# Optimization experiments

Hardware: AMD Instinct MI355X
Metric: run time of the kernel (lower is better)

Reference implementation:

```python
import jax, jax.numpy as jnp
import numpy as np

B, T, C, A, P = 16, 1024, 512, 4096, 256  # batch, frames, phones, allophone arcs, phonemes


def setup_inputs() -> dict:
    key = jax.random.key(0)
    k1, k2, k3 = jax.random.split(key, 3)
    hs_pad = jax.random.normal(k1, (B, T, C), dtype=jnp.float32)
    # each phone has exactly A // C allophone arcs (full coverage, balanced)
    phone_arc_labels = jnp.arange(A, dtype=jnp.int32) % C
    arcs_per_phone = A // C
    # weights near -log(arcs_per_phone) so sum_a exp(log_prob + w) ~= 1,
    # matching a trained allophone layer and keeping the redis step log-safe
    alloW = 0.01 * jax.random.normal(k2, (A,), dtype=jnp.float32) - jnp.log(
        jnp.float32(arcs_per_phone)
    )
    phoneme_arc_labels = jax.random.randint(k3, (A,), 0, P, dtype=jnp.int32)
    return {
        "hs_pad": hs_pad,
        "alloW": alloW,
        "phone_arc_labels": phone_arc_labels,
        "phoneme_arc_labels": phoneme_arc_labels,
        "n_phonemes": P,
    }


def reference(hs_pad, alloW, phone_arc_labels, phoneme_arc_labels, n_phonemes):
    # log_softmax over phones
    log_probs = jax.nn.log_softmax(hs_pad, axis=-1)  # [B,T,C]
    # WFST intersection of linear emission graph with 1-state allophone graph:
    # arc a gets weight log_probs[..., phone_label(a)] + alloW[a]
    new_emissions = log_probs[..., phone_arc_labels] + alloW  # [B,T,A]
    # squash many phones per phoneme: exp + scatter-add over output labels
    ex = jnp.exp(new_emissions)
    Bq, Tq = ex.shape[0], ex.shape[1]
    squashed = jnp.zeros((Bq, Tq, n_phonemes), dtype=ex.dtype)
    squashed = squashed.at[..., phoneme_arc_labels].add(ex)  # [B,T,P]
    # redistribute probability mass so it sums to 1
    redistributed = (squashed.sum(axis=-1) - 1.0)[..., None] / n_phonemes
    squashed = squashed - redistributed
    return jnp.log(squashed)
```

## Files before the change

### kernel.cpp

```cpp
#include <hip/hip_runtime.h>
#include <hip/hip_bf16.h>

#define BT   16384
#define CDIM 512
#define ADIM 4096
#define PDIM 256

typedef __attribute__((ext_vector_type(8))) short short8;
typedef __attribute__((ext_vector_type(4))) float f32x4;

__device__ __forceinline__ unsigned short bf16_rne(float f) {
    unsigned int u = __float_as_uint(f);
    u += 0x7FFFu + ((u >> 16) & 1u);
    return (unsigned short)(u >> 16);
}

__global__ __launch_bounds__(256) void build_Wf(const float* __restrict__ alloW,
                                                const int* __restrict__ phone_lab,
                                                const int* __restrict__ phoneme_lab,
                                                unsigned short* __restrict__ Wf) {
    __shared__ float wrow[PDIM];
    const int c = blockIdx.x;
    const int t = threadIdx.x;
    wrow[t] = 0.0f;
    __syncthreads();
#pragma unroll
    for (int i = 0; i < ADIM / 256; ++i) {
        int a = i * 256 + t;
        if (phone_lab[a] == c)
            atomicAdd(&wrow[phoneme_lab[a]], __expf(alloW[a]));
    }
    __syncthreads();
    Wf[(c >> 5) * (PDIM * 32) + t * 32 + (c & 31)] = bf16_rne(wrow[t]);
}

__global__ __launch_bounds__(256) void allo_fused(const float* __restrict__ hs,
                                                  const unsigned short* __restrict__ Wf,
                                                  float* __restrict__ out) {
    __shared__ __align__(16) unsigned short Af[2 * 16 * 16 * 32];
    __shared__ float invZ[32];
    __shared__ float psum[4][32];

    const int tid  = threadIdx.x;
    const int row0 = blockIdx.x * 32;

    {
        const int r   = tid >> 3;
        const int ksl = tid & 7;
        const int rb  = r >> 4;
        const int cc  = r & 15;
        const float* hsr = hs + (size_t)(row0 + r) * CDIM + ksl * 4;
        unsigned short* af = Af + rb * 8192 + cc * 32 + ksl * 4;

        float s = 0.0f;
#pragma unroll
        for (int i = 0; i < 16; ++i) {
            float4 v = *(const float4*)(hsr + i * 32);
            float e0 = __expf(v.x), e1 = __expf(v.y);
            float e2 = __expf(v.z), e3 = __expf(v.w);
            s += (e0 + e1) + (e2 + e3);
            ushort4 pk;
            pk.x = bf16_rne(e0); pk.y = bf16_rne(e1);
            pk.z = bf16_rne(e2); pk.w = bf16_rne(e3);
            *(ushort4*)(af + i * 512) = pk;
        }
        s += __shfl_xor(s, 1);
        s += __shfl_xor(s, 2);
        s += __shfl_xor(s, 4);
        if (ksl == 0) invZ[r] = 1.0f / s;
    }
    __syncthreads();

    const int wave = tid >> 6;
    const int lane = tid & 63;
    const int c    = lane & 15;
    const int q    = lane >> 4;

    f32x4 acc[2][4];
#pragma unroll
    for (int rb = 0; rb < 2; ++rb)
#pragma unroll
        for (int cb = 0; cb < 4; ++cb)
            acc[rb][cb] = (f32x4){0.f, 0.f, 0.f, 0.f};

    const unsigned short* wb  = Wf + (size_t)(wave * 64 + c) * 32 + q * 8;
    const unsigned short* af0 = Af + c * 32 + q * 8;

#pragma unroll 4
    for (int kb = 0; kb < 16; ++kb) {
        short8 a0 = *(const short8*)(af0 + kb * 512);
        short8 a1 = *(const short8*)(af0 + 8192 + kb * 512);

        const unsigned short* wkb = wb + kb * 8192;
        short8 b0 = *(const short8*)(wkb);
        short8 b1 = *(const short8*)(wkb + 512);
        short8 b2 = *(const short8*)(wkb + 1024);
        short8 b3 = *(const short8*)(wkb + 1536);

        acc[0][0] = __builtin_amdgcn_mfma_f32_16x16x32_bf16(a0, b0, acc[0][0], 0, 0, 0);
        acc[0][1] = __builtin_amdgcn_mfma_f32_16x16x32_bf16(a0, b1, acc[0][1], 0, 0, 0);
        acc[0][2] = __builtin_amdgcn_mfma_f32_16x16x32_bf16(a0, b2, acc[0][2], 0, 0, 0);
        acc[0][3] = __builtin_amdgcn_mfma_f32_16x16x32_bf16(a0, b3, acc[0][3], 0, 0, 0);
        acc[1][0] = __builtin_amdgcn_mfma_f32_16x16x32_bf16(a1, b0, acc[1][0], 0, 0, 0);
        acc[1][1] = __builtin_amdgcn_mfma_f32_16x16x32_bf16(a1, b1, acc[1][1], 0, 0, 0);
        acc[1][2] = __builtin_amdgcn_mfma_f32_16x16x32_bf16(a1, b2, acc[1][2], 0, 0, 0);
        acc[1][3] = __builtin_amdgcn_mfma_f32_16x16x32_bf16(a1, b3, acc[1][3], 0, 0, 0);
    }

    float s[2][4];
#pragma unroll
    for (int rb = 0; rb < 2; ++rb)
#pragma unroll
        for (int r = 0; r < 4; ++r) {
            float v = acc[rb][0][r] + acc[rb][1][r] + acc[rb][2][r] + acc[rb][3][r];
            v += __shfl_xor(v, 1);
            v += __shfl_xor(v, 2);
            v += __shfl_xor(v, 4);
            v += __shfl_xor(v, 8);
            s[rb][r] = v;
        }
    if (c == 0) {
#pragma unroll
        for (int rb = 0; rb < 2; ++rb)
#pragma unroll
            for (int r = 0; r < 4; ++r)
                psum[wave][rb * 16 + q * 4 + r] = s[rb][r];
    }
    __syncthreads();

#pragma unroll
    for (int rb = 0; rb < 2; ++rb)
#pragma unroll
        for (int r = 0; r < 4; ++r) {
            const int rr  = rb * 16 + q * 4 + r;
            const float iz = invZ[rr];
            const float S  = (psum[0][rr] + psum[1][rr] + psum[2][rr] + psum[3][rr]) * iz;
            const float corr = (S - 1.0f) * (1.0f / (float)PDIM);
            float* orow = out + (size_t)(row0 + rr) * PDIM + wave * 64 + c;
#pragma unroll
            for (int cb = 0; cb < 4; ++cb)
                orow[cb * 16] = __logf(acc[rb][cb][r] * iz - corr);
        }
}

extern "C" void kernel_launch(void* const* d_in, const int* in_sizes, int n_in,
                              void* d_out, int out_size, void* d_ws, size_t ws_size,
                              hipStream_t stream) {
    const float* hs          = (const float*)d_in[0];
    const float* alloW       = (const float*)d_in[1];
    const int*   phone_lab   = (const int*)d_in[2];
    const int*   phoneme_lab = (const int*)d_in[3];
    float*       out         = (float*)d_out;

    unsigned short* Wf = (unsigned short*)d_ws;

    build_Wf<<<CDIM, 256, 0, stream>>>(alloW, phone_lab, phoneme_lab, Wf);
    allo_fused<<<BT / 32, 256, 0, stream>>>(hs, Wf, out);
}
```

Baseline: 99.15 us.

## Halve rows per block, spread exp prologue across waves, batch Wf build

The main kernel now handles 16 rows per block instead of 32, which doubles the grid to 1024 blocks. The exp/bf16 prologue is split so each wave handles a quarter of the K range with 8-wide vector stores, and partial row sums are combined through shared-memory atomics. build_Wf now builds 32 phone columns per block with vectorized 16-byte stores, cutting that launch from 512 blocks to 16. The intent is more parallelism and occupancy (launch bounds 256,4). In exchange, each Wf tile fetched from global or L2 is reused across half as many rows, so global traffic on the weight matrix doubles.

```diff
diff --git a/kernel.cpp b/kernel.cpp
--- a/kernel.cpp
+++ b/kernel.cpp
@@ -6,8 +6,9 @@
 #define ADIM 4096
 #define PDIM 256
 
-typedef __attribute__((ext_vector_type(8))) short short8;
-typedef __attribute__((ext_vector_type(4))) float f32x4;
+typedef __attribute__((ext_vector_type(8))) short  short8;
+typedef __attribute__((ext_vector_type(8))) unsigned short ushort8;
+typedef __attribute__((ext_vector_type(4))) float  f32x4;
 
 __device__ __forceinline__ unsigned short bf16_rne(float f) {
     unsigned int u = __float_as_uint(f);
@@ -19,69 +20,87 @@
                                                 const int* __restrict__ phone_lab,
                                                 const int* __restrict__ phoneme_lab,
                                                 unsigned short* __restrict__ Wf) {
-    __shared__ float wrow[PDIM];
-    const int c = blockIdx.x;
-    const int t = threadIdx.x;
-    wrow[t] = 0.0f;
+    __shared__ float wrow[32 * PDIM];
+    const int bx = blockIdx.x;
+    const int t  = threadIdx.x;
+
+#pragma unroll
+    for (int i = 0; i < 32; ++i) wrow[i * 256 + t] = 0.0f;
     __syncthreads();
+
 #pragma unroll
     for (int i = 0; i < ADIM / 256; ++i) {
         int a = i * 256 + t;
-        if (phone_lab[a] == c)
-            atomicAdd(&wrow[phoneme_lab[a]], __expf(alloW[a]));
+        int c = phone_lab[a];
+        if ((c >> 5) == bx)
+            atomicAdd(&wrow[(c & 31) * 256 + phoneme_lab[a]], __expf(alloW[a]));
     }
     __syncthreads();
-    Wf[(c >> 5) * (PDIM * 32) + t * 32 + (c & 31)] = bf16_rne(wrow[t]);
+
+    ushort8 pk[4];
+#pragma unroll
+    for (int g = 0; g < 4; ++g) {
+#pragma unroll
+        for (int j = 0; j < 8; ++j)
+            pk[g][j] = bf16_rne(wrow[(g * 8 + j) * 256 + t]);
+    }
+    unsigned short* dst = Wf + (size_t)bx * (PDIM * 32) + t * 32;
+#pragma unroll
+    for (int g = 0; g < 4; ++g)
+        *(ushort8*)(dst + g * 8) = pk[g];
 }
 
-__global__ __launch_bounds__(256) void allo_fused(const float* __restrict__ hs,
-                                                  const unsigned short* __restrict__ Wf,
-                                                  float* __restrict__ out) {
-    __shared__ __align__(16) unsigned short Af[2 * 16 * 16 * 32];
-    __shared__ float invZ[32];
-    __shared__ float psum[4][32];
+__global__ __launch_bounds__(256, 4) void allo_fused(const float* __restrict__ hs,
+                                                     const unsigned short* __restrict__ Wf,
+                                                     float* __restrict__ out) {
+    __shared__ __align__(16) unsigned short Af[16 * 512];
+    __shared__ float sZ[16];
+    __shared__ float psum[4][16];
 
     const int tid  = threadIdx.x;
-    const int row0 = blockIdx.x * 32;
+    const int wave = tid >> 6;
+    const int lane = tid & 63;
+    const int row0 = blockIdx.x * 16;
+
+    if (tid < 16) sZ[tid] = 0.0f;
+    __syncthreads();
 
     {
-        const int r   = tid >> 3;
-        const int ksl = tid & 7;
-        const int rb  = r >> 4;
-        const int cc  = r & 15;
-        const float* hsr = hs + (size_t)(row0 + r) * CDIM + ksl * 4;
-        unsigned short* af = Af + rb * 8192 + cc * 32 + ksl * 4;
+        const int pc = lane >> 2;
+        const int pj = lane & 3;
+        const float* hsr = hs + (size_t)(row0 + pc) * CDIM + pj * 8;
+        unsigned short* af = Af + pc * 32 + pj * 8;
 
         float s = 0.0f;
 #pragma unroll
-        for (int i = 0; i < 16; ++i) {
-            float4 v = *(const float4*)(hsr + i * 32);
-            float e0 = __expf(v.x), e1 = __expf(v.y);
-            float e2 = __expf(v.z), e3 = __expf(v.w);
-            s += (e0 + e1) + (e2 + e3);
-            ushort4 pk;
-            pk.x = bf16_rne(e0); pk.y = bf16_rne(e1);
-            pk.z = bf16_rne(e2); pk.w = bf16_rne(e3);
-            *(ushort4*)(af + i * 512) = pk;
+        for (int i = 0; i < 4; ++i) {
+            const int kb = wave * 4 + i;
+            float4 v0 = *(const float4*)(hsr + kb * 32);
+            float4 v1 = *(const float4*)(hsr + kb * 32 + 4);
+            float e0 = __expf(v0.x), e1 = __expf(v0.y);
+            float e2 = __expf(v0.z), e3 = __expf(v0.w);
+            float e4 = __expf(v1.x), e5 = __expf(v1.y);
+            float e6 = __expf(v1.z), e7 = __expf(v1.w);
+            s += ((e0 + e1) + (e2 + e3)) + ((e4 + e5) + (e6 + e7));
+            ushort8 pk;
+            pk[0] = bf16_rne(e0); pk[1] = bf16_rne(e1);
+            pk[2] = bf16_rne(e2); pk[3] = bf16_rne(e3);
+            pk[4] = bf16_rne(e4); pk[5] = bf16_rne(e5);
+            pk[6] = bf16_rne(e6); pk[7] = bf16_rne(e7);
+            *(ushort8*)(af + kb * 512) = pk;
         }
         s += __shfl_xor(s, 1);
         s += __shfl_xor(s, 2);
-        s += __shfl_xor(s, 4);
-        if (ksl == 0) invZ[r] = 1.0f / s;
+        if (pj == 0) atomicAdd(&sZ[pc], s);
     }
     __syncthreads();
 
-    const int wave = tid >> 6;
-    const int lane = tid & 63;
-    const int c    = lane & 15;
-    const int q    = lane >> 4;
+    const int c = lane & 15;
+    const int q = lane >> 4;
 
-    f32x4 acc[2][4];
+    f32x4 acc[4];
 #pragma unroll
-    for (int rb = 0; rb < 2; ++rb)
-#pragma unroll
-        for (int cb = 0; cb < 4; ++cb)
-            acc[rb][cb] = (f32x4){0.f, 0.f, 0.f, 0.f};
+    for (int cb = 0; cb < 4; ++cb) acc[cb] = (f32x4){0.f, 0.f, 0.f, 0.f};
 
     const unsigned short* wb  = Wf + (size_t)(wave * 64 + c) * 32 + q * 8;
     const unsigned short* af0 = Af + c * 32 + q * 8;
@@ -89,58 +108,47 @@
 #pragma unroll 4
     for (int kb = 0; kb < 16; ++kb) {
         short8 a0 = *(const short8*)(af0 + kb * 512);
-        short8 a1 = *(const short8*)(af0 + 8192 + kb * 512);
-
         const unsigned short* wkb = wb + kb * 8192;
         short8 b0 = *(const short8*)(wkb);
         short8 b1 = *(const short8*)(wkb + 512);
         short8 b2 = *(const short8*)(wkb + 1024);
         short8 b3 = *(const short8*)(wkb + 1536);
 
-        acc[0][0] = __builtin_amdgcn_mfma_f32_16x16x32_bf16(a0, b0, acc[0][0], 0, 0, 0);
-        acc[0][1] = __builtin_amdgcn_mfma_f32_16x16x32_bf16(a0, b1, acc[0][1], 0, 0, 0);
-        acc[0][2] = __builtin_amdgcn_mfma_f32_16x16x32_bf16(a0, b2, acc[0][2], 0, 0, 0);
-        acc[0][3] = __builtin_amdgcn_mfma_f32_16x16x32_bf16(a0, b3, acc[0][3], 0, 0, 0);
-        acc[1][0] = __builtin_amdgcn_mfma_f32_16x16x32_bf16(a1, b0, acc[1][0], 0, 0, 0);
-        acc[1][1] = __builtin_amdgcn_mfma_f32_16x16x32_bf16(a1, b1, acc[1][1], 0, 0, 0);
-        acc[1][2] = __builtin_amdgcn_mfma_f32_16x16x32_bf16(a1, b2, acc[1][2], 0, 0, 0);
-        acc[1][3] = __builtin_amdgcn_mfma_f32_16x16x32_bf16(a1, b3, acc[1][3], 0, 0, 0);
+        acc[0] = __builtin_amdgcn_mfma_f32_16x16x32_bf16(a0, b0, acc[0], 0, 0, 0);
+        acc[1] = __builtin_amdgcn_mfma_f32_16x16x32_bf16(a0, b1, acc[1], 0, 0, 0);
+        acc[2] = __builtin_amdgcn_mfma_f32_16x16x32_bf16(a0, b2, acc[2], 0, 0, 0);
+        acc[3] = __builtin_amdgcn_mfma_f32_16x16x32_bf16(a0, b3, acc[3], 0, 0, 0);
     }
 
-    float s[2][4];
-#pragma unroll
-    for (int rb = 0; rb < 2; ++rb)
+    {
+        float v[4];
 #pragma unroll
         for (int r = 0; r < 4; ++r) {
-            float v = acc[rb][0][r] + acc[rb][1][r] + acc[rb][2][r] + acc[rb][3][r];
-            v += __shfl_xor(v, 1);
-            v += __shfl_xor(v, 2);
-            v += __shfl_xor(v, 4);
-            v += __shfl_xor(v, 8);
-            s[rb][r] = v;
+            float x = (acc[0][r] + acc[1][r]) + (acc[2][r] + acc[3][r]);
+            x += __shfl_xor(x, 1);
+            x += __shfl_xor(x, 2);
+            x += __shfl_xor(x, 4);
+            x += __shfl_xor(x, 8);
+            v[r] = x;
         }
-    if (c == 0) {
+        if (c == 0) {
 #pragma unroll
-        for (int rb = 0; rb < 2; ++rb)
-#pragma unroll
-            for (int r = 0; r < 4; ++r)
-                psum[wave][rb * 16 + q * 4 + r] = s[rb][r];
+            for (int r = 0; r < 4; ++r) psum[wave][q * 4 + r] = v[r];
+        }
     }
     __syncthreads();
 
 #pragma unroll
-    for (int rb = 0; rb < 2; ++rb)
+    for (int r = 0; r < 4; ++r) {
+        const int rr = q * 4 + r;
+        const float iz = 1.0f / sZ[rr];
+        const float S  = ((psum[0][rr] + psum[1][rr]) + (psum[2][rr] + psum[3][rr])) * iz;
+        const float corr = (S - 1.0f) * (1.0f / (float)PDIM);
+        float* orow = out + (size_t)(row0 + rr) * PDIM + wave * 64 + c;
 #pragma unroll
-        for (int r = 0; r < 4; ++r) {
-            const int rr  = rb * 16 + q * 4 + r;
-            const float iz = invZ[rr];
-            const float S  = (psum[0][rr] + psum[1][rr] + psum[2][rr] + psum[3][rr]) * iz;
-            const float corr = (S - 1.0f) * (1.0f / (float)PDIM);
-            float* orow = out + (size_t)(row0 + rr) * PDIM + wave * 64 + c;
-#pragma unroll
-            for (int cb = 0; cb < 4; ++cb)
-                orow[cb * 16] = __logf(acc[rb][cb][r] * iz - corr);
-        }
+        for (int cb = 0; cb < 4; ++cb)
+            orow[cb * 16] = __logf(acc[cb][r] * iz - corr);
+    }
 }
 
 extern "C" void kernel_launch(void* const* d_in, const int* in_sizes, int n_in,
@@ -154,6 +162,6 @@
 
     unsigned short* Wf = (unsigned short*)d_ws;
 
-    build_Wf<<<CDIM, 256, 0, stream>>>(alloW, phone_lab, phoneme_lab, Wf);
-    allo_fused<<<BT / 32, 256, 0, stream>>>(hs, Wf, out);
+    build_Wf<<<CDIM / 32, 256, 0, stream>>>(alloW, phone_lab, phoneme_lab, Wf);
+    allo_fused<<<BT / 16, 256, 0, stream>>>(hs, Wf, out);
 }
```

After: 107.4 us. 1.08x slower.

## Batch Wf build per 32 phones and double-buffer MFMA operand loads

Applied to the files above, without the earlier changes.

build_Wf now runs 16 blocks, each building 32 phone rows in shared memory and writing them with vectorized 16-byte stores, where before 512 blocks each wrote scattered 2-byte values. The main kernel splits the exp/bf16 staging into two batches of eight float4 loads to expose memory-level parallelism. Its MFMA loop is register double-buffered, prefetching the next two k-steps of A and B while the current ones compute. A min-blocks-per-CU hint of 2 is added. The build kernel now uses far fewer blocks, and the prefetch buffers raise register pressure.

```diff
diff --git a/kernel.cpp b/kernel.cpp
--- a/kernel.cpp
+++ b/kernel.cpp
@@ -6,8 +6,9 @@
 #define ADIM 4096
 #define PDIM 256
 
-typedef __attribute__((ext_vector_type(8))) short short8;
-typedef __attribute__((ext_vector_type(4))) float f32x4;
+typedef __attribute__((ext_vector_type(8))) short  short8;
+typedef __attribute__((ext_vector_type(8))) unsigned short ushort8;
+typedef __attribute__((ext_vector_type(4))) float  f32x4;
 
 __device__ __forceinline__ unsigned short bf16_rne(float f) {
     unsigned int u = __float_as_uint(f);
@@ -19,29 +20,46 @@
                                                 const int* __restrict__ phone_lab,
                                                 const int* __restrict__ phoneme_lab,
                                                 unsigned short* __restrict__ Wf) {
-    __shared__ float wrow[PDIM];
-    const int c = blockIdx.x;
-    const int t = threadIdx.x;
-    wrow[t] = 0.0f;
-    __syncthreads();
+    __shared__ float wrow[32 * PDIM];
+    const int bx = blockIdx.x;
+    const int t  = threadIdx.x;
+
+#pragma unroll
+    for (int i = 0; i < 32; ++i) wrow[i * 256 + t] = 0.0f;
+    __syncthreads();
+
 #pragma unroll
     for (int i = 0; i < ADIM / 256; ++i) {
         int a = i * 256 + t;
-        if (phone_lab[a] == c)
-            atomicAdd(&wrow[phoneme_lab[a]], __expf(alloW[a]));
-    }
-    __syncthreads();
-    Wf[(c >> 5) * (PDIM * 32) + t * 32 + (c & 31)] = bf16_rne(wrow[t]);
-}
-
-__global__ __launch_bounds__(256) void allo_fused(const float* __restrict__ hs,
-                                                  const unsigned short* __restrict__ Wf,
-                                                  float* __restrict__ out) {
+        int c = phone_lab[a];
+        if ((c >> 5) == bx)
+            atomicAdd(&wrow[(c & 31) * 256 + phoneme_lab[a]], __expf(alloW[a]));
+    }
+    __syncthreads();
+
+    ushort8 pk[4];
+#pragma unroll
+    for (int g = 0; g < 4; ++g) {
+#pragma unroll
+        for (int j = 0; j < 8; ++j)
+            pk[g][j] = bf16_rne(wrow[(g * 8 + j) * 256 + t]);
+    }
+    unsigned short* dst = Wf + (size_t)bx * (PDIM * 32) + t * 32;
+#pragma unroll
+    for (int g = 0; g < 4; ++g)
+        *(ushort8*)(dst + g * 8) = pk[g];
+}
+
+__global__ __launch_bounds__(256, 2) void allo_fused(const float* __restrict__ hs,
+                                                     const unsigned short* __restrict__ Wf,
+                                                     float* __restrict__ out) {
     __shared__ __align__(16) unsigned short Af[2 * 16 * 16 * 32];
     __shared__ float invZ[32];
     __shared__ float psum[4][32];
 
     const int tid  = threadIdx.x;
+    const int wave = tid >> 6;
+    const int lane = tid & 63;
     const int row0 = blockIdx.x * 32;
 
     {
@@ -54,15 +72,21 @@
 
         float s = 0.0f;
 #pragma unroll
-        for (int i = 0; i < 16; ++i) {
-            float4 v = *(const float4*)(hsr + i * 32);
-            float e0 = __expf(v.x), e1 = __expf(v.y);
-            float e2 = __expf(v.z), e3 = __expf(v.w);
-            s += (e0 + e1) + (e2 + e3);
-            ushort4 pk;
-            pk.x = bf16_rne(e0); pk.y = bf16_rne(e1);
-            pk.z = bf16_rne(e2); pk.w = bf16_rne(e3);
-            *(ushort4*)(af + i * 512) = pk;
+        for (int h = 0; h < 2; ++h) {
+            float4 v[8];
+#pragma unroll
+            for (int i = 0; i < 8; ++i)
+                v[i] = *(const float4*)(hsr + (h * 8 + i) * 32);
+#pragma unroll
+            for (int i = 0; i < 8; ++i) {
+                float e0 = __expf(v[i].x), e1 = __expf(v[i].y);
+                float e2 = __expf(v[i].z), e3 = __expf(v[i].w);
+                s += (e0 + e1) + (e2 + e3);
+                ushort4 pk;
+                pk.x = bf16_rne(e0); pk.y = bf16_rne(e1);
+                pk.z = bf16_rne(e2); pk.w = bf16_rne(e3);
+                *(ushort4*)(af + (h * 8 + i) * 512) = pk;
+            }
         }
         s += __shfl_xor(s, 1);
         s += __shfl_xor(s, 2);
@@ -71,10 +95,8 @@
     }
     __syncthreads();
 
-    const int wave = tid >> 6;
-    const int lane = tid & 63;
-    const int c    = lane & 15;
-    const int q    = lane >> 4;
+    const int c = lane & 15;
+    const int q = lane >> 4;
 
     f32x4 acc[2][4];
 #pragma unroll
@@ -86,45 +108,64 @@
     const unsigned short* wb  = Wf + (size_t)(wave * 64 + c) * 32 + q * 8;
     const unsigned short* af0 = Af + c * 32 + q * 8;
 
-#pragma unroll 4
-    for (int kb = 0; kb < 16; ++kb) {
-        short8 a0 = *(const short8*)(af0 + kb * 512);
-        short8 a1 = *(const short8*)(af0 + 8192 + kb * 512);
-
-        const unsigned short* wkb = wb + kb * 8192;
-        short8 b0 = *(const short8*)(wkb);
-        short8 b1 = *(const short8*)(wkb + 512);
-        short8 b2 = *(const short8*)(wkb + 1024);
-        short8 b3 = *(const short8*)(wkb + 1536);
-
-        acc[0][0] = __builtin_amdgcn_mfma_f32_16x16x32_bf16(a0, b0, acc[0][0], 0, 0, 0);
-        acc[0][1] = __builtin_amdgcn_mfma_f32_16x16x32_bf16(a0, b1, acc[0][1], 0, 0, 0);
-        acc[0][2] = __builtin_amdgcn_mfma_f32_16x16x32_bf16(a0, b2, acc[0][2], 0, 0, 0);
-        acc[0][3] = __builtin_amdgcn_mfma_f32_16x16x32_bf16(a0, b3, acc[0][3], 0, 0, 0);
-        acc[1][0] = __builtin_amdgcn_mfma_f32_16x16x32_bf16(a1, b0, acc[1][0], 0, 0, 0);
-        acc[1][1] = __builtin_amdgcn_mfma_f32_16x16x32_bf16(a1, b1, acc[1][1], 0, 0, 0);
-        acc[1][2] = __builtin_amdgcn_mfma_f32_16x16x32_bf16(a1, b2, acc[1][2], 0, 0, 0);
-        acc[1][3] = __builtin_amdgcn_mfma_f32_16x16x32_bf16(a1, b3, acc[1][3], 0, 0, 0);
-    }
-
-    float s[2][4];
+    short8 Bb[2][2][4];
+    short8 Ab[2][2][2];
+
+#pragma unroll
+    for (int it = 0; it < 2; ++it) {
+        const unsigned short* wkb = wb + it * 8192;
+#pragma unroll
+        for (int cb = 0; cb < 4; ++cb)
+            Bb[0][it][cb] = *(const short8*)(wkb + cb * 512);
+#pragma unroll
+        for (int rb = 0; rb < 2; ++rb)
+            Ab[0][it][rb] = *(const short8*)(af0 + rb * 8192 + it * 512);
+    }
+
+#pragma unroll
+    for (int g = 0; g < 8; ++g) {
+        const int cur = g & 1, nxt = cur ^ 1;
+        if (g < 7) {
+            const int kb0 = (g + 1) * 2;
+#pragma unroll
+            for (int it = 0; it < 2; ++it) {
+                const unsigned short* wkb = wb + (size_t)(kb0 + it) * 8192;
+#pragma unroll
+                for (int cb = 0; cb < 4; ++cb)
+                    Bb[nxt][it][cb] = *(const short8*)(wkb + cb * 512);
+#pragma unroll
+                for (int rb = 0; rb < 2; ++rb)
+                    Ab[nxt][it][rb] = *(const short8*)(af0 + rb * 8192 + (kb0 + it) * 512);
+            }
+        }
+#pragma unroll
+        for (int it = 0; it < 2; ++it)
+#pragma unroll
+            for (int rb = 0; rb < 2; ++rb)
+#pragma unroll
+                for (int cb = 0; cb < 4; ++cb)
+                    acc[rb][cb] = __builtin_amdgcn_mfma_f32_16x16x32_bf16(
+                        Ab[cur][it][rb], Bb[cur][it][cb], acc[rb][cb], 0, 0, 0);
+    }
+
+    float sv[2][4];
 #pragma unroll
     for (int rb = 0; rb < 2; ++rb)
 #pragma unroll
         for (int r = 0; r < 4; ++r) {
-            float v = acc[rb][0][r] + acc[rb][1][r] + acc[rb][2][r] + acc[rb][3][r];
-            v += __shfl_xor(v, 1);
-            v += __shfl_xor(v, 2);
-            v += __shfl_xor(v, 4);
-            v += __shfl_xor(v, 8);
-            s[rb][r] = v;
+            float x = (acc[rb][0][r] + acc[rb][1][r]) + (acc[rb][2][r] + acc[rb][3][r]);
+            x += __shfl_xor(x, 1);
+            x += __shfl_xor(x, 2);
+            x += __shfl_xor(x, 4);
+            x += __shfl_xor(x, 8);
+            sv[rb][r] = x;
         }
     if (c == 0) {
 #pragma unroll
         for (int rb = 0; rb < 2; ++rb)
 #pragma unroll
             for (int r = 0; r < 4; ++r)
-                psum[wave][rb * 16 + q * 4 + r] = s[rb][r];
+                psum[wave][rb * 16 + q * 4 + r] = sv[rb][r];
     }
     __syncthreads();
 
@@ -132,9 +173,9 @@
     for (int rb = 0; rb < 2; ++rb)
 #pragma unroll
         for (int r = 0; r < 4; ++r) {
-            const int rr  = rb * 16 + q * 4 + r;
+            const int rr = rb * 16 + q * 4 + r;
             const float iz = invZ[rr];
-            const float S  = (psum[0][rr] + psum[1][rr] + psum[2][rr] + psum[3][rr]) * iz;
+            const float S  = ((psum[0][rr] + psum[1][rr]) + (psum[2][rr] + psum[3][rr])) * iz;
             const float corr = (S - 1.0f) * (1.0f / (float)PDIM);
             float* orow = out + (size_t)(row0 + rr) * PDIM + wave * 64 + c;
 #pragma unroll
@@ -154,6 +195,6 @@
 
     unsigned short* Wf = (unsigned short*)d_ws;
 
-    build_Wf<<<CDIM, 256, 0, stream>>>(alloW, phone_lab, phoneme_lab, Wf);
+    build_Wf<<<CDIM / 32, 256, 0, stream>>>(alloW, phone_lab, phoneme_lab, Wf);
     allo_fused<<<BT / 32, 256, 0, stream>>>(hs, Wf, out);
 }
```

Measured after the change: 100.2 us. Within noise of the previous version (+1.0%).
